# Performance work log

Hardware: AMD Instinct MI355X
Metric: run time of the kernel (lower is better)

Reference implementation:

```python
import jax, jax.numpy as jnp
import numpy as np

NSAMPLES = 30
TOPK = 32
EPS = 1e-8


def setup_inputs() -> dict:
    key = jax.random.key(0)
    k1, k2 = jax.random.split(key)
    B, N, C, S = 4, 4096, 256, 256
    x = jax.random.normal(k1, (B, N, C), dtype=jnp.float32)
    # affinity matrix (B, num_spixels, N); strictly positive weights for multinomial
    amatrix = jax.random.uniform(k2, (B, S, N), dtype=jnp.float32)
    return {"x": x, "amatrix": amatrix, "num_spixels": S}


def _exact_attn(x, sims, indices, labels):
    # x: (B,N,C); sims/indices: (B,S,K) topk affinities / pixel ids per superpixel
    # labels: (B,N) sampled superpixel id per pixel
    C = x.shape[-1]
    # per-pixel gather of its sampled superpixel's top-K member pixels
    idx = jnp.take_along_axis(indices, labels[:, :, None], axis=1)   # (B,N,K)
    w = jnp.take_along_axis(sims, labels[:, :, None], axis=1)        # (B,N,K)
    keys = jax.vmap(lambda xb, ib: xb[ib])(x, idx)                   # (B,N,K,C)
    scores = jnp.einsum('bnc,bnkc->bnk', x, keys) / jnp.sqrt(jnp.float32(C))
    attn = jax.nn.softmax(scores + jnp.log(w + EPS), axis=-1)        # (B,N,K)
    return jnp.einsum('bnk,bnkc->bnc', attn, keys)


def reference(x, amatrix, num_spixels):
    # topk over candidate-pixel axis, once (torch.topk(amatrix, topk, dim=-1))
    sims, indices = jax.lax.top_k(amatrix, TOPK)                     # (B,S,K)
    # multinomial(amatrix.T): sample a superpixel per pixel from its affinity column
    logits = jnp.log(amatrix + EPS).transpose(0, 2, 1)               # (B,N,S)
    sample_keys = jax.random.split(jax.random.key(1), NSAMPLES)

    def body(acc, k):
        labels = jax.random.categorical(k, logits, axis=-1)          # (B,N)
        acc = acc + _exact_attn(x, sims, indices, labels) / NSAMPLES
        return acc, None

    out, _ = jax.lax.scan(body, jnp.zeros_like(x), sample_keys)
    return out
```

## Files before the change

### kernel.cpp

```cpp
#include <hip/hip_runtime.h>
#include <hip/hip_bf16.h>


#define BB 4
#define NN 4096
#define CC 256
#define SS 256
#define KKK 32
#define NSAMP 30
#define NBIN (BB*SS)
#define TOTQ (NSAMP*BB*NN)

typedef _Float16 half8 __attribute__((ext_vector_type(8)));
typedef _Float16 half4v __attribute__((ext_vector_type(4)));
typedef float f32x4 __attribute__((ext_vector_type(4)));

struct Keys30 { unsigned k0[NSAMP]; unsigned k1[NSAMP]; };

__host__ __device__ __forceinline__ void threefry2x32(unsigned k0, unsigned k1,
    unsigned x0, unsigned x1, unsigned& o0, unsigned& o1) {
  unsigned ks2 = k0 ^ k1 ^ 0x1BD11BDAu;
#define TFROT(r) { x0 += x1; x1 = __builtin_rotateleft32(x1, (r)); x1 ^= x0; }
  x0 += k0; x1 += k1;
  TFROT(13) TFROT(15) TFROT(26) TFROT(6)
  x0 += k1;  x1 += ks2 + 1u;
  TFROT(17) TFROT(29) TFROT(16) TFROT(24)
  x0 += ks2; x1 += k0 + 2u;
  TFROT(13) TFROT(15) TFROT(26) TFROT(6)
  x0 += k0;  x1 += k1 + 3u;
  TFROT(17) TFROT(29) TFROT(16) TFROT(24)
  x0 += k1;  x1 += ks2 + 4u;
  TFROT(13) TFROT(15) TFROT(26) TFROT(6)
  x0 += ks2; x1 += k0 + 5u;
#undef TFROT
  o0 = x0; o1 = x1;
}

__device__ __forceinline__ float uniform_from_bits(unsigned bits) {
  float u = __uint_as_float((bits >> 9) | 0x3f800000u) - 1.0f;
  return fmaxf(u, 1.17549435e-38f);
}

__device__ __forceinline__ float gumbel_exact(unsigned bits) {
  float u = uniform_from_bits(bits);
  return -logf(-logf(u));
}

__global__ __launch_bounds__(256) void invw_kernel(const float* __restrict__ am,
                                                   float* __restrict__ nw) {
  int i = (blockIdx.x * 256 + threadIdx.x) << 2;
  float4 v = *(const float4*)&am[i];
  float4 o;
  o.x = -1.0f / (v.x + 1e-8f); o.y = -1.0f / (v.y + 1e-8f);
  o.z = -1.0f / (v.z + 1e-8f); o.w = -1.0f / (v.w + 1e-8f);
  *(float4*)&nw[i] = o;
}

__global__ __launch_bounds__(256) void topk_kernel(const float* __restrict__ am,
                                                   int* __restrict__ indices,
                                                   float* __restrict__ logw) {
  __shared__ float vals[NN];
  __shared__ float wv[4];
  __shared__ int   wi[4];
  const int row = blockIdx.x;
  const int tid = threadIdx.x;
  const float* src = am + (size_t)row * NN;
  for (int i = tid; i < NN; i += 256) vals[i] = src[i];
  __syncthreads();
  for (int k = 0; k < KKK; ++k) {
    float bv = -INFINITY; int bi = -1;
    #pragma unroll
    for (int j = 0; j < NN / 256; ++j) {
      int idx = tid + j * 256;
      float v = vals[idx];
      if (v > bv) { bv = v; bi = idx; }
    }
    #pragma unroll
    for (int off = 32; off; off >>= 1) {
      float ov = __shfl_down(bv, off);
      int   oi = __shfl_down(bi, off);
      if (ov > bv || (ov == bv && oi < bi)) { bv = ov; bi = oi; }
    }
    if ((tid & 63) == 0) { wv[tid >> 6] = bv; wi[tid >> 6] = bi; }
    __syncthreads();
    if (tid == 0) {
      bv = wv[0]; bi = wi[0];
      for (int w = 1; w < 4; ++w)
        if (wv[w] > bv || (wv[w] == bv && wi[w] < bi)) { bv = wv[w]; bi = wi[w]; }
      indices[row * KKK + k] = bi;
      logw[row * KKK + k] = logf(bv + 1e-8f);
      vals[bi] = -INFINITY;
    }
    __syncthreads();
  }
}

__global__ __launch_bounds__(256) void sample_top2_kernel(
    const float* __restrict__ ninvw, const float* __restrict__ am,
    unsigned char* __restrict__ labels, Keys30 keys) {
  const int t0 = blockIdx.x * 256 + threadIdx.x;
  const int n = t0 & (NN - 1);
  const int b = (t0 >> 12) & 3;
  const int samp = t0 >> 14;
  const unsigned k0 = keys.k0[samp], k1 = keys.k1[samp];
  const unsigned jbase = ((unsigned)((b << 12) + n)) << 8;
  const float* wcol = ninvw + ((size_t)(b << 8)) * NN + n;

  float r1 = INFINITY, r2 = INFINITY;
  int   i1 = 0;
  #pragma unroll 8
  for (int s = 0; s < SS; ++s) {
    unsigned o0, o1;
    threefry2x32(k0, k1, 0u, jbase + (unsigned)s, o0, o1);
    float u = uniform_from_bits(o0 ^ o1);
    float r = __builtin_amdgcn_logf(u) * wcol[(size_t)s * NN];
    bool better = r < r1;
    r2 = better ? r1 : fminf(r2, r);
    r1 = better ? r  : r1;
    i1 = better ? s  : i1;
  }
  bool uncert = !(r2 > r1 * 1.0001f);
  if (__ballot(uncert)) {
    if (uncert) {
      const float* acol = am + ((size_t)(b << 8)) * NN + n;
      float best = -INFINITY; int bi = 0;
      for (int s = 0; s < SS; ++s) {
        unsigned o0, o1;
        threefry2x32(k0, k1, 0u, jbase + (unsigned)s, o0, o1);
        float tot = gumbel_exact(o0 ^ o1) + logf(acol[(size_t)s * NN] + 1e-8f);
        if (tot > best) { best = tot; bi = s; }
      }
      i1 = bi;
    }
  }
  labels[((samp << 2) + b) * NN + n] = (unsigned char)i1;
}

__global__ __launch_bounds__(256) void hist_kernel(const unsigned char* __restrict__ lbl,
                                                   int* __restrict__ hist) {
  __shared__ int h[NBIN];
  for (int i = threadIdx.x; i < NBIN; i += 256) h[i] = 0;
  __syncthreads();
  for (int e = blockIdx.x * 256 + threadIdx.x; e < TOTQ; e += gridDim.x * 256) {
    int bgrp = (e >> 12) & 3;
    atomicAdd(&h[(bgrp << 8) + lbl[e]], 1);
  }
  __syncthreads();
  for (int i = threadIdx.x; i < NBIN; i += 256) if (h[i]) atomicAdd(&hist[i], h[i]);
}

__global__ __launch_bounds__(1024) void scan_kernel(const int* __restrict__ hist,
                                                    int* __restrict__ binstart,
                                                    int* __restrict__ cursor) {
  __shared__ int a[NBIN];
  const int tid = threadIdx.x;
  const int h = hist[tid];
  a[tid] = h;
  __syncthreads();
  for (int off = 1; off < NBIN; off <<= 1) {
    int v = (tid >= off) ? a[tid - off] : 0;
    __syncthreads();
    a[tid] += v;
    __syncthreads();
  }
  int excl = a[tid] - h;
  binstart[tid] = excl;
  cursor[tid]   = excl;
}

__global__ __launch_bounds__(256) void scatter_kernel(const unsigned char* __restrict__ lbl,
                                                      int* __restrict__ cursor,
                                                      int* __restrict__ qlist) {
  for (int e = blockIdx.x * 256 + threadIdx.x; e < TOTQ; e += gridDim.x * 256) {
    int bgrp = (e >> 12) & 3;
    int bin = (bgrp << 8) + lbl[e];
    int slot = atomicAdd(&cursor[bin], 1);
    qlist[slot] = e & (NN - 1);
  }
}

__global__ __launch_bounds__(256, 2) void attn_mfma_kernel(
    const float* __restrict__ x, const int* __restrict__ indices,
    const float* __restrict__ logw, const int* __restrict__ qlist,
    const int* __restrict__ binstart, const int* __restrict__ hist,
    float* __restrict__ out) {
  __shared__ _Float16 Qlds[64 * 256];
  __shared__ _Float16 Klds[32 * 256];
  __shared__ _Float16 KT[256 * 40];
  __shared__ _Float16 Plds[4 * 16 * 32];
  __shared__ int   kidx_s[KKK];
  __shared__ float kbias_s[KKK];

  const int tid = threadIdx.x;
  const int b = blockIdx.x & 3;
  const int s = blockIdx.x >> 2;
  const int bin = (b << 8) + s;
  const int base = binstart[bin];
  const int cnt  = hist[bin];

  if (tid < KKK) {
    int r = bin * KKK + tid;
    kidx_s[tid]  = indices[r];
    kbias_s[tid] = logw[r];
  }
  __syncthreads();

  const int w = tid >> 6, lane = tid & 63;
  const int qr = lane & 15, kg = lane >> 4;

  {
    const int c4 = (lane) << 2;
    #pragma unroll
    for (int p = 0; p < 8; ++p) {
      int r = (p << 2) + w;
      const float4 v = *(const float4*)&x[((size_t)((b << 12) + kidx_s[r]) << 8) + c4];
      half4v h;
      h[0] = (_Float16)v.x; h[1] = (_Float16)v.y;
      h[2] = (_Float16)v.z; h[3] = (_Float16)v.w;
      *(half4v*)&Klds[(r << 8) + (c4 ^ ((r & 7) << 3))] = h;
      KT[(c4 + 0) * 40 + r] = h[0];
      KT[(c4 + 1) * 40 + r] = h[1];
      KT[(c4 + 2) * 40 + r] = h[2];
      KT[(c4 + 3) * 40 + r] = h[3];
    }
  }

  const int nchunk = (cnt + 63) >> 6;
  for (int chk = 0; chk < nchunk; ++chk) {
    const int rmax = min(64, cnt - (chk << 6));
    __syncthreads();
    {
      const int c4 = lane << 2;
      #pragma unroll
      for (int p = 0; p < 16; ++p) {
        int r = (p << 2) + w;
        int rr = min(r, rmax - 1);
        int n = qlist[base + (chk << 6) + rr];
        const float4 v = *(const float4*)&x[((size_t)((b << 12) + n) << 8) + c4];
        half4v h;
        h[0] = (_Float16)v.x; h[1] = (_Float16)v.y;
        h[2] = (_Float16)v.z; h[3] = (_Float16)v.w;
        *(half4v*)&Qlds[(r << 8) + (c4 ^ ((r & 7) << 3))] = h;
      }
    }
    __syncthreads();

    f32x4 acc0 = {0.f, 0.f, 0.f, 0.f}, acc1 = {0.f, 0.f, 0.f, 0.f};
    {
      const int arow = (w << 4) + qr;
      const _Float16* Arow = &Qlds[arow << 8];
      const int asz = (arow & 7) << 3;
      const _Float16* B0 = &Klds[qr << 8];
      const _Float16* B1 = &Klds[(16 + qr) << 8];
      const int bsz = (qr & 7) << 3;
      #pragma unroll
      for (int kk = 0; kk < 8; ++kk) {
        const int off = (kk << 5) + (kg << 3);
        half8 a  = *(const half8*)&Arow[off ^ asz];
        half8 b0 = *(const half8*)&B0[off ^ bsz];
        half8 b1 = *(const half8*)&B1[off ^ bsz];
        acc0 = __builtin_amdgcn_mfma_f32_16x16x32_f16(a, b0, acc0, 0, 0, 0);
        acc1 = __builtin_amdgcn_mfma_f32_16x16x32_f16(a, b1, acc1, 0, 0, 0);
      }
    }
    {
      const float b0v = kbias_s[qr], b1v = kbias_s[16 + qr];
      #pragma unroll
      for (int r = 0; r < 4; ++r) {
        float s0 = acc0[r] * 0.0625f + b0v;
        float s1 = acc1[r] * 0.0625f + b1v;
        float m = fmaxf(s0, s1);
        #pragma unroll
        for (int o = 1; o < 16; o <<= 1) m = fmaxf(m, __shfl_xor(m, o));
        float e0 = __expf(s0 - m), e1 = __expf(s1 - m);
        float sm = e0 + e1;
        #pragma unroll
        for (int o = 1; o < 16; o <<= 1) sm += __shfl_xor(sm, o);
        float inv = 1.0f / sm;
        int prow = (kg << 2) + r;
        _Float16* P = &Plds[(w << 9) + (prow << 5)];
        P[qr]      = (_Float16)(e0 * inv);
        P[16 + qr] = (_Float16)(e1 * inv);
      }
    }
    __builtin_amdgcn_wave_barrier();
    {
      half8 a2 = *(const half8*)&Plds[(w << 9) + (qr << 5) + (kg << 3)];
      int nr[4];
      #pragma unroll
      for (int r = 0; r < 4; ++r) {
        int grow = (w << 4) + (kg << 2) + r;
        nr[r] = (grow < rmax) ? qlist[base + (chk << 6) + grow] : -1;
      }
      #pragma unroll
      for (int t = 0; t < 16; ++t) {
        half8 bb = *(const half8*)&KT[((t << 4) + qr) * 40 + (kg << 3)];
        f32x4 zero = {0.f, 0.f, 0.f, 0.f};
        f32x4 o = __builtin_amdgcn_mfma_f32_16x16x32_f16(a2, bb, zero, 0, 0, 0);
        #pragma unroll
        for (int r = 0; r < 4; ++r) {
          if (nr[r] >= 0)
            atomicAdd(&out[((size_t)((b << 12) + nr[r]) << 8) + (t << 4) + qr],
                      o[r] * (1.0f / 30.0f));
        }
      }
    }
  }
}

#define OFF_IDX   0
#define OFF_LOGW  131072
#define OFF_LBL   262144
#define OFF_NW    786432
#define OFF_HIST  17563648
#define OFF_BST   17567744
#define OFF_CUR   17571840
#define OFF_QL    17575936

extern "C" void kernel_launch(void* const* d_in, const int* in_sizes, int n_in,
                              void* d_out, int out_size, void* d_ws, size_t ws_size,
                              hipStream_t stream) {
  const float* x  = (const float*)d_in[0];
  const float* am = (const float*)d_in[1];
  float* out = (float*)d_out;

  char* ws = (char*)d_ws;
  int*   indices = (int*)(ws + OFF_IDX);
  float* logw    = (float*)(ws + OFF_LOGW);
  unsigned char* labels = (unsigned char*)(ws + OFF_LBL);
  float* ninvw   = (float*)(ws + OFF_NW);
  int*   hist    = (int*)(ws + OFF_HIST);
  int*   binstart= (int*)(ws + OFF_BST);
  int*   cursor  = (int*)(ws + OFF_CUR);
  int*   qlist   = (int*)(ws + OFF_QL);

  Keys30 keys;
  for (int s = 0; s < NSAMP; ++s) {
    unsigned o0, o1;
    threefry2x32(0u, 1u, 0u, (unsigned)s, o0, o1);
    keys.k0[s] = o0; keys.k1[s] = o1;
  }

  hipMemsetAsync(d_out, 0, (size_t)out_size * 4, stream);
  hipMemsetAsync(hist, 0, NBIN * 4, stream);

  invw_kernel<<<(BB * SS * NN) / (256 * 4), 256, 0, stream>>>(am, ninvw);
  topk_kernel<<<BB * SS, 256, 0, stream>>>(am, indices, logw);
  sample_top2_kernel<<<TOTQ / 256, 256, 0, stream>>>(ninvw, am, labels, keys);
  hist_kernel<<<240, 256, 0, stream>>>(labels, hist);
  scan_kernel<<<1, 1024, 0, stream>>>(hist, binstart, cursor);
  scatter_kernel<<<240, 256, 0, stream>>>(labels, cursor, qlist);
  attn_mfma_kernel<<<NBIN, 256, 0, stream>>>(x, indices, logw, qlist, binstart,
                                             hist, out);
}
```

Measured before the change: 1.047 ms.

## Split sampling loop into two independent halves and prune exact fallback candidates

The per-pixel Gumbel-max sampling loop now runs two independent chains over the two halves of the superpixel range, which gives the compiler more instruction-level parallelism across threefry hashing and loads. The top-2 tracking is rewritten with branchless min/max, and the block size drops to 64 threads. The exact fallback path now skips the costly exact Gumbel and log for candidates whose fast approximate score is clearly above the best. This adds register pressure, and the pruning margin has to keep the fallback exact.

```diff
diff --git a/kernel.cpp b/kernel.cpp
--- a/kernel.cpp
+++ b/kernel.cpp
@@ -95,10 +95,10 @@
   }
 }
 
-__global__ __launch_bounds__(256) void sample_top2_kernel(
+__global__ __launch_bounds__(64) void sample_ilp2_kernel(
     const float* __restrict__ ninvw, const float* __restrict__ am,
     unsigned char* __restrict__ labels, Keys30 keys) {
-  const int t0 = blockIdx.x * 256 + threadIdx.x;
+  const int t0 = blockIdx.x * 64 + threadIdx.x;
   const int n = t0 & (NN - 1);
   const int b = (t0 >> 12) & 3;
   const int samp = t0 >> 14;
@@ -106,29 +106,49 @@
   const unsigned jbase = ((unsigned)((b << 12) + n)) << 8;
   const float* wcol = ninvw + ((size_t)(b << 8)) * NN + n;
 
-  float r1 = INFINITY, r2 = INFINITY;
-  int   i1 = 0;
-  #pragma unroll 8
-  for (int s = 0; s < SS; ++s) {
-    unsigned o0, o1;
+  float r1a = INFINITY, r2a = INFINITY; int i1a = 0;
+  float r1b = INFINITY, r2b = INFINITY; int i1b = 128;
+  const float* pa = wcol;
+  const float* pb = wcol + (size_t)128 * NN;
+  #pragma unroll 4
+  for (int s = 0; s < 128; ++s) {
+    unsigned o0, o1, q0, q1;
     threefry2x32(k0, k1, 0u, jbase + (unsigned)s, o0, o1);
-    float u = uniform_from_bits(o0 ^ o1);
-    float r = __builtin_amdgcn_logf(u) * wcol[(size_t)s * NN];
-    bool better = r < r1;
-    r2 = better ? r1 : fminf(r2, r);
-    r1 = better ? r  : r1;
-    i1 = better ? s  : i1;
-  }
+    threefry2x32(k0, k1, 0u, jbase + (unsigned)(s + 128), q0, q1);
+    float ua = uniform_from_bits(o0 ^ o1);
+    float ub = uniform_from_bits(q0 ^ q1);
+    float ra = __builtin_amdgcn_logf(ua) * (*pa);
+    float rb = __builtin_amdgcn_logf(ub) * (*pb);
+    pa += NN; pb += NN;
+    bool ba = ra < r1a;
+    r2a = fminf(r2a, fmaxf(ra, r1a));
+    r1a = fminf(r1a, ra);
+    i1a = ba ? s : i1a;
+    bool bb = rb < r1b;
+    r2b = fminf(r2b, fmaxf(rb, r1b));
+    r1b = fminf(r1b, rb);
+    i1b = bb ? (s + 128) : i1b;
+  }
+  bool bwin = r1b < r1a;
+  float r1 = bwin ? r1b : r1a;
+  int   i1 = bwin ? i1b : i1a;
+  float r2 = fminf(fmaxf(r1a, r1b), fminf(r2a, r2b));
+
   bool uncert = !(r2 > r1 * 1.0001f);
   if (__ballot(uncert)) {
     if (uncert) {
       const float* acol = am + ((size_t)(b << 8)) * NN + n;
+      const float lim = r1 * 1.0002f;
       float best = -INFINITY; int bi = 0;
       for (int s = 0; s < SS; ++s) {
         unsigned o0, o1;
         threefry2x32(k0, k1, 0u, jbase + (unsigned)s, o0, o1);
-        float tot = gumbel_exact(o0 ^ o1) + logf(acol[(size_t)s * NN] + 1e-8f);
-        if (tot > best) { best = tot; bi = s; }
+        float u = uniform_from_bits(o0 ^ o1);
+        float r = __builtin_amdgcn_logf(u) * wcol[(size_t)s * NN];
+        if (r <= lim) {
+          float tot = gumbel_exact(o0 ^ o1) + logf(acol[(size_t)s * NN] + 1e-8f);
+          if (tot > best) { best = tot; bi = s; }
+        }
       }
       i1 = bi;
     }
@@ -346,7 +366,7 @@
 
   invw_kernel<<<(BB * SS * NN) / (256 * 4), 256, 0, stream>>>(am, ninvw);
   topk_kernel<<<BB * SS, 256, 0, stream>>>(am, indices, logw);
-  sample_top2_kernel<<<TOTQ / 256, 256, 0, stream>>>(ninvw, am, labels, keys);
+  sample_ilp2_kernel<<<TOTQ / 64, 64, 0, stream>>>(ninvw, am, labels, keys);
   hist_kernel<<<240, 256, 0, stream>>>(labels, hist);
   scan_kernel<<<1, 1024, 0, stream>>>(hist, binstart, cursor);
   scatter_kernel<<<240, 256, 0, stream>>>(labels, cursor, qlist);
```

Result: faster. 1.017 ms (-2.8%).
